# Optimization experiments

Hardware: AMD Instinct MI355X
Metric: run time of the kernel (lower is better)

The kernel has to match this reference:

```python
import jax, jax.numpy as jnp
import numpy as np

B, D, NH, NL, NP, DFF = 2, 256, 8, 4, 4, 1024
HD = D // NH
SHAPES = [(128, 128), (64, 64), (32, 32), (16, 16)]  # (H, W) per level
S = sum(h * w for h, w in SHAPES)  # 21760
EPS = 1e-5


def _layer_norm(x, g, b):
    m = jnp.mean(x, -1, keepdims=True)
    v = jnp.mean(jnp.square(x - m), -1, keepdims=True)
    return (x - m) * jax.lax.rsqrt(v + EPS) * g + b


def _bilinear(v, grid, Hl, Wl):
    # v: [B, Hl*Wl, NH, HD]; grid: [B, S, NH, NP, 2] in [0,1] (x,y)
    # grid_sample semantics, align_corners=False, zero padding
    x = grid[..., 0] * Wl - 0.5
    y = grid[..., 1] * Hl - 0.5
    x0 = jnp.floor(x); y0 = jnp.floor(y)
    dx = x - x0; dy = y - y0
    x0i = x0.astype(jnp.int32); y0i = y0.astype(jnp.int32)

    def corner(xi, yi, w):
        valid = (xi >= 0) & (xi < Wl) & (yi >= 0) & (yi < Hl)
        idx = jnp.clip(yi, 0, Hl - 1) * Wl + jnp.clip(xi, 0, Wl - 1)  # [B,S,NH,NP]
        g_hw = lambda vb, ib: vb[ib]  # [HW,HD],[S,NP] -> [S,NP,HD]
        gat = jax.vmap(jax.vmap(g_hw, in_axes=(1, 1), out_axes=1))(v, idx)  # [B,S,NH,NP,HD]
        return gat * (w * valid.astype(v.dtype))[..., None]

    return (corner(x0i, y0i, (1 - dx) * (1 - dy))
            + corner(x0i + 1, y0i, dx * (1 - dy))
            + corner(x0i, y0i + 1, (1 - dx) * dy)
            + corner(x0i + 1, y0i + 1, dx * dy))


def _ms_deform_attn(query, value_in, ref_pts, shapes,
                    W_off, b_off, W_attn, b_attn, W_val, b_val, W_out, b_out):
    Bq, Sq = query.shape[:2]
    value = (value_in @ W_val + b_val).reshape(Bq, Sq, NH, HD)
    off = (query @ W_off + b_off).reshape(Bq, Sq, NH, NL, NP, 2)
    aw = (query @ W_attn + b_attn).reshape(Bq, Sq, NH, NL * NP)
    aw = jax.nn.softmax(aw, axis=-1).reshape(Bq, Sq, NH, NL, NP)
    # offset normalizer is (W, H) per level
    norm = jnp.array([[w, h] for h, w in shapes], dtype=query.dtype)
    loc = ref_pts[:, :, None, :, None, :] + off / norm[None, None, None, :, None, :]
    out = jnp.zeros((Bq, Sq, NH, HD), query.dtype)
    start = 0
    for l, (Hl, Wl) in enumerate(shapes):
        v_l = value[:, start:start + Hl * Wl]
        sampled = _bilinear(v_l, loc[:, :, :, l], Hl, Wl)  # [B,S,NH,NP,HD]
        out = out + jnp.einsum('bqhp,bqhpd->bqhd', aw[:, :, :, l], sampled)
        start += Hl * Wl
    return out.reshape(Bq, Sq, D) @ W_out + b_out


def setup_inputs() -> dict:
    key = jax.random.key(0)
    ks = jax.random.split(key, 16)
    sc = 0.02
    lsi = np.cumsum([0] + [h * w for h, w in SHAPES[:-1]])
    return dict(
        src=jax.random.normal(ks[0], (B, S, D), jnp.float32),
        pos=jax.random.normal(ks[1], (B, S, D), jnp.float32),
        reference_points=jax.random.uniform(ks[2], (B, S, NL, 2), jnp.float32),
        spatial_shapes=jnp.array(SHAPES, jnp.int32),
        level_start_index=jnp.array(lsi, jnp.int32),
        W_off=sc * jax.random.normal(ks[3], (D, NH * NL * NP * 2), jnp.float32),
        b_off=jnp.zeros((NH * NL * NP * 2,), jnp.float32),
        W_attn=sc * jax.random.normal(ks[4], (D, NH * NL * NP), jnp.float32),
        b_attn=jnp.zeros((NH * NL * NP,), jnp.float32),
        W_val=sc * jax.random.normal(ks[5], (D, D), jnp.float32),
        b_val=jnp.zeros((D,), jnp.float32),
        W_out=sc * jax.random.normal(ks[6], (D, D), jnp.float32),
        b_out=jnp.zeros((D,), jnp.float32),
        g1=jnp.ones((D,), jnp.float32), be1=jnp.zeros((D,), jnp.float32),
        W_ff1=sc * jax.random.normal(ks[7], (D, DFF), jnp.float32),
        b_ff1=jnp.zeros((DFF,), jnp.float32),
        W_ff2=sc * jax.random.normal(ks[8], (DFF, D), jnp.float32),
        b_ff2=jnp.zeros((D,), jnp.float32),
        g2=jnp.ones((D,), jnp.float32), be2=jnp.zeros((D,), jnp.float32),
    )


def reference(src, pos, reference_points, spatial_shapes, level_start_index,
              W_off, b_off, W_attn, b_attn, W_val, b_val, W_out, b_out,
              g1, be1, W_ff1, b_ff1, W_ff2, b_ff2, g2, be2):
    # spatial_shapes is static metadata (defines per-level reshapes)
    shapes = [tuple(int(v) for v in row) for row in np.asarray(spatial_shapes)]
    attn = _ms_deform_attn(src + pos, src, reference_points, shapes,
                           W_off, b_off, W_attn, b_attn, W_val, b_val, W_out, b_out)
    x = _layer_norm(src + attn, g1, be1)
    ffn = jax.nn.relu(x @ W_ff1 + b_ff1) @ W_ff2 + b_ff2
    return _layer_norm(x + ffn, g2, be2)
```

## Files before the change

kernel.cpp:

```cpp
#include <hip/hip_runtime.h>
#include <cstdint>
#include <cstddef>

#define B_   2
#define S_   21760
#define M_   (B_ * S_)
#define D_   256
#define DFF_ 1024
#define EPS_ 1e-5f

typedef __attribute__((ext_vector_type(8))) short short8;
typedef __attribute__((ext_vector_type(4))) float f32x4;
typedef __attribute__((ext_vector_type(2))) float f32x2;

__device__ __forceinline__ ushort f2bf(float f) {
    uint x = __float_as_uint(f);
    return (ushort)((x + 0x7fffu + ((x >> 16) & 1u)) >> 16);
}
__device__ __forceinline__ float bf2f(ushort u) {
    return __uint_as_float(((uint)u) << 16);
}

#define CVT_BLOCKS 10880
__global__ __launch_bounds__(256) void prep_all(
    const float* __restrict__ src, const float* __restrict__ pos,
    ushort* __restrict__ sb, ushort* __restrict__ qb,
    const float* __restrict__ Wval, const float* __restrict__ Woff,
    const float* __restrict__ Wattn, const float* __restrict__ Wout,
    const float* __restrict__ Wff1, const float* __restrict__ Wff2,
    const float* __restrict__ boff, const float* __restrict__ battn,
    ushort* __restrict__ WT, float* __restrict__ bias_oa)
{
    if (blockIdx.x < CVT_BLOCKS) {
        const size_t i = ((size_t)blockIdx.x * 256 + threadIdx.x) * 4;
        const float4 s = *(const float4*)(src + i);
        const float4 p = *(const float4*)(pos + i);
        ushort4 so, qo;
        so.x = f2bf(s.x); so.y = f2bf(s.y); so.z = f2bf(s.z); so.w = f2bf(s.w);
        qo.x = f2bf(s.x + p.x); qo.y = f2bf(s.y + p.y);
        qo.z = f2bf(s.z + p.z); qo.w = f2bf(s.w + p.w);
        *(ushort4*)(sb + i) = so;
        *(ushort4*)(qb + i) = qo;
        return;
    }
    const int i = (blockIdx.x - CVT_BLOCKS) * 256 + threadIdx.x;
    if (i < 65536) {
        const int n = i >> 8, k = i & 255;
        WT[i] = f2bf(Wval[(size_t)k * 256 + n]);
    } else if (i < 163840) {
        const int j = i - 65536;
        const int n = j >> 8, k = j & 255;
        WT[i] = (n < 256) ? f2bf(Woff[(size_t)k * 256 + n])
                          : f2bf(Wattn[(size_t)k * 128 + (n - 256)]);
    } else if (i < 229376) {
        const int j = i - 163840;
        const int n = j >> 8, k = j & 255;
        WT[i] = f2bf(Wout[(size_t)k * 256 + n]);
    } else if (i < 491520) {
        const int j = i - 229376;
        const int n = j >> 8, k = j & 255;
        WT[i] = f2bf(Wff1[(size_t)k * 1024 + n]);
    } else if (i < 753664) {
        const int j = i - 491520;
        const int n = j >> 10, k = j & 1023;
        WT[i] = f2bf(Wff2[(size_t)k * 256 + n]);
    } else if (i < 753664 + 384) {
        const int j = i - 753664;
        bias_oa[j] = (j < 256) ? boff[j] : battn[j - 256];
    }
}

__global__ __launch_bounds__(256) void mgemm(
    const ushort* __restrict__ A, const ushort* __restrict__ WT,
    const float* __restrict__ bias, ushort* __restrict__ C,
    int M, int N, int K, int relu, int mode)
{
    __shared__ __align__(16) ushort Als[128 * 64];
    __shared__ __align__(16) ushort Bls[128 * 64];

    const int nwg = gridDim.x;
    const int bid = blockIdx.x;
    const int q8 = nwg >> 3, r8 = nwg & 7;
    const int xcd = bid & 7, blk = bid >> 3;
    const int wg = (xcd < r8 ? xcd * (q8 + 1) : r8 * (q8 + 1) + (xcd - r8) * q8) + blk;
    const int gx = N >> 7;
    const int n0 = (wg % gx) << 7;
    const int m0 = (wg / gx) << 7;

    const int tid = threadIdx.x;
    const int wv = tid >> 6, ln = tid & 63;
    const int wm = wv >> 1, wn = wv & 1;

    const int srow = ln >> 3;
    const int scol = ((ln & 7) ^ srow) * 8;

    f32x4 acc[4][4];
    const f32x4 zz = {0.f, 0.f, 0.f, 0.f};
    #pragma unroll
    for (int i = 0; i < 4; i++)
        #pragma unroll
        for (int j = 0; j < 4; j++) acc[i][j] = zz;

    const int fr = ln & 15, qq = ln >> 4;

    for (int k0 = 0; k0 < K; k0 += 64) {
        __syncthreads();
        #pragma unroll
        for (int r = 0; r < 4; ++r) {
            const int c = r * 4 + wv;
            const ushort* ga = A + (size_t)(m0 + c * 8 + srow) * K + k0 + scol;
            __builtin_amdgcn_global_load_lds(
                (const __attribute__((address_space(1))) uint*)ga,
                (__attribute__((address_space(3))) uint*)(Als + c * 512), 16, 0, 0);
            const ushort* gb = WT + (size_t)(n0 + c * 8 + srow) * K + k0 + scol;
            __builtin_amdgcn_global_load_lds(
                (const __attribute__((address_space(1))) uint*)gb,
                (__attribute__((address_space(3))) uint*)(Bls + c * 512), 16, 0, 0);
        }
        __syncthreads();

        #pragma unroll
        for (int kk = 0; kk < 2; kk++) {
            short8 af[4], bfr[4];
            #pragma unroll
            for (int i = 0; i < 4; i++) {
                const int row = wm * 64 + i * 16 + fr;
                af[i] = *(const short8*)&Als[row * 64 + (((kk * 4 + qq) ^ (row & 7)) * 8)];
            }
            #pragma unroll
            for (int j = 0; j < 4; j++) {
                const int row = wn * 64 + j * 16 + fr;
                bfr[j] = *(const short8*)&Bls[row * 64 + (((kk * 4 + qq) ^ (row & 7)) * 8)];
            }
            #pragma unroll
            for (int i = 0; i < 4; i++)
                #pragma unroll
                for (int j = 0; j < 4; j++)
                    acc[i][j] = __builtin_amdgcn_mfma_f32_16x16x32_bf16(
                        af[i], bfr[j], acc[i][j], 0, 0, 0);
        }
    }

    uint8_t* C8 = (uint8_t*)C;
    const int rq = (ln >> 4) * 4;
    #pragma unroll
    for (int j = 0; j < 4; j++) {
        const int col = n0 + wn * 64 + j * 16 + fr;
        const float bv = bias[col];
        #pragma unroll
        for (int i = 0; i < 4; i++) {
            #pragma unroll
            for (int r = 0; r < 4; r++) {
                const int row = m0 + wm * 64 + i * 16 + rq + r;
                float v = acc[i][j][r] + bv;
                if (relu) v = fmaxf(v, 0.f);
                if (mode == 0) {
                    C[(size_t)row * N + col] = f2bf(v);
                } else {
                    const int bb = (row >= S_) ? 1 : 0;
                    const int loc = row - bb * S_;
                    const int hh = col >> 5, ch = col & 31;
                    const int pk = __builtin_amdgcn_cvt_pk_fp8_f32(v, v, 0, false);
                    C8[((size_t)(bb * 8 + hh) * S_ + loc) * 32 + ch] = (uint8_t)(pk & 0xff);
                }
            }
        }
    }
}

__global__ __launch_bounds__(256) void ln_row(
    const ushort* __restrict__ a16, const ushort* __restrict__ r16,
    const float* __restrict__ g, const float* __restrict__ be,
    float* __restrict__ o32, ushort* __restrict__ o16)
{
    const int wv = threadIdx.x >> 6, ln = threadIdx.x & 63;
    const int row = blockIdx.x * 4 + wv;
    const int col = ln * 4;
    const size_t base = (size_t)row * 256 + col;

    const ushort4 av = *(const ushort4*)(a16 + base);
    const ushort4 rv = *(const ushort4*)(r16 + base);
    float v0 = bf2f(av.x) + bf2f(rv.x);
    float v1 = bf2f(av.y) + bf2f(rv.y);
    float v2 = bf2f(av.z) + bf2f(rv.z);
    float v3 = bf2f(av.w) + bf2f(rv.w);

    float s = v0 + v1 + v2 + v3;
    float s2 = v0 * v0 + v1 * v1 + v2 * v2 + v3 * v3;
    #pragma unroll
    for (int o = 32; o > 0; o >>= 1) {
        s  += __shfl_down(s, o);
        s2 += __shfl_down(s2, o);
    }
    s = __shfl(s, 0);
    s2 = __shfl(s2, 0);
    const float mean = s * (1.f / 256.f);
    const float var = s2 * (1.f / 256.f) - mean * mean;
    const float rstd = rsqrtf(var + EPS_);

    const float4 gv = *(const float4*)(g + col);
    const float4 bv = *(const float4*)(be + col);
    const float o0 = (v0 - mean) * rstd * gv.x + bv.x;
    const float o1 = (v1 - mean) * rstd * gv.y + bv.y;
    const float o2 = (v2 - mean) * rstd * gv.z + bv.z;
    const float o3 = (v3 - mean) * rstd * gv.w + bv.w;

    if (o32) {
        float4 o; o.x = o0; o.y = o1; o.z = o2; o.w = o3;
        *(float4*)(o32 + base) = o;
    } else {
        ushort4 o; o.x = f2bf(o0); o.y = f2bf(o1); o.z = f2bf(o2); o.w = f2bf(o3);
        *(ushort4*)(o16 + base) = o;
    }
}

__global__ __launch_bounds__(256) void sample8(
    const uint8_t* __restrict__ value, const ushort* __restrict__ offaw,
    const float* __restrict__ refp, ushort* __restrict__ samp)
{
    const int bid = blockIdx.x;
    const int wg = (bid & 7) * 680 + (bid >> 3);
    const int bh = wg / 340;
    const int qc = wg - bh * 340;
    const int b = bh >> 3, h = bh & 7;

    const int tid = threadIdx.x;
    const int g = tid >> 2, cg = tid & 3;
    const int q = b * S_ + qc * 64 + g;
    const int half = cg >> 1;
    const int gbase = (tid & 63) & ~3;

    const int Wl = 128 >> cg;
    const float fW = (float)Wl;
    const int st = (cg == 0) ? 0 : (cg == 1) ? 16384 : (cg == 2) ? 20480 : 21504;

    const ushort* awq = offaw + (size_t)q * 384 + 256 + h * 16 + cg * 4;
    const uint2 lg = *(const uint2*)awq;
    const float l0 = bf2f((ushort)(lg.x & 0xffff)), l1 = bf2f((ushort)(lg.x >> 16));
    const float l2 = bf2f((ushort)(lg.y & 0xffff)), l3 = bf2f((ushort)(lg.y >> 16));
    float mx = fmaxf(fmaxf(l0, l1), fmaxf(l2, l3));
    mx = fmaxf(mx, __shfl_xor(mx, 1));
    mx = fmaxf(mx, __shfl_xor(mx, 2));
    const float e0 = __expf(l0 - mx), e1 = __expf(l1 - mx);
    const float e2 = __expf(l2 - mx), e3 = __expf(l3 - mx);
    float sm = e0 + e1 + e2 + e3;
    sm += __shfl_xor(sm, 1);
    sm += __shfl_xor(sm, 2);
    const float inv = 1.f / sm;
    const float aj[4] = {e0 * inv, e1 * inv, e2 * inv, e3 * inv};

    const ushort* ofq = offaw + (size_t)q * 384 + h * 32 + cg * 8;
    const uint4 of = *(const uint4*)ofq;
    const uint ou[4] = {of.x, of.y, of.z, of.w};
    const float rx = refp[(size_t)q * 8 + cg * 2];
    const float ry = refp[(size_t)q * 8 + cg * 2 + 1];

    int  rxo[8];
    uint wpk[8];
    #pragma unroll
    for (int j = 0; j < 4; j++) {
        const float ox = bf2f((ushort)(ou[j] & 0xffff));
        const float oy = bf2f((ushort)(ou[j] >> 16));
        const float x = fmaf(rx, fW, ox) - 0.5f;
        const float y = fmaf(ry, fW, oy) - 0.5f;
        const float fx0 = floorf(x), fy0 = floorf(y);
        const float dx = x - fx0, dy = y - fy0;
        const int x0 = (int)fx0, y0 = (int)fy0;

        const int bx = min(max(x0, 0), Wl - 2);
        const float mwx0 = ((x0 >= 0) & (x0 < Wl)) ? (1.f - dx) : 0.f;
        const float mwx1 = ((x0 + 1 >= 0) & (x0 + 1 < Wl)) ? dx : 0.f;
        const int xc0 = min(max(x0, 0), Wl - 1);
        const int xc1 = min(max(x0 + 1, 0), Wl - 1);
        const float wAx = (xc0 == bx ? mwx0 : 0.f) + (xc1 == bx ? mwx1 : 0.f);
        const float wBx = (xc0 == bx + 1 ? mwx0 : 0.f) + (xc1 == bx + 1 ? mwx1 : 0.f);

        const int yc0 = min(max(y0, 0), Wl - 1);
        const int yc1 = min(max(y0 + 1, 0), Wl - 1);
        const float mwy0 = ((y0 >= 0) & (y0 < Wl)) ? (1.f - dy) : 0.f;
        const float mwy1 = ((y0 + 1 >= 0) & (y0 + 1 < Wl)) ? dy : 0.f;

        const float a = aj[j];
        rxo[2 * j]     = (st + yc0 * Wl + bx) * 32;
        rxo[2 * j + 1] = (st + yc1 * Wl + bx) * 32;
        wpk[2 * j]     = (uint)f2bf(a * wAx * mwy0) | ((uint)f2bf(a * wBx * mwy0) << 16);
        wpk[2 * j + 1] = (uint)f2bf(a * wAx * mwy1) | ((uint)f2bf(a * wBx * mwy1) << 16);
    }

    const uint8_t* vb = value + (size_t)(b * 8 + h) * S_ * 32 + cg * 16;
    f32x2 acc[8];
    #pragma unroll
    for (int k = 0; k < 8; k++) acc[k] = (f32x2){0.f, 0.f};

    #pragma unroll
    for (int ol = 0; ol < 4; ol++) {
        const int srcl = gbase + ol;
        #pragma unroll
        for (int r = 0; r < 8; r++) {
            const int  rix = __shfl(rxo[r], srcl, 64);
            const uint wp  = (uint)__shfl((int)wpk[r], srcl, 64);
            const float wv = bf2f((ushort)(half ? (wp >> 16) : (wp & 0xffffu)));
            const uint4 u = *(const uint4*)(vb + rix);
            const f32x2 w2 = {wv, wv};
            acc[0] += w2 * __builtin_amdgcn_cvt_pk_f32_fp8((int)u.x, false);
            acc[1] += w2 * __builtin_amdgcn_cvt_pk_f32_fp8((int)u.x, true);
            acc[2] += w2 * __builtin_amdgcn_cvt_pk_f32_fp8((int)u.y, false);
            acc[3] += w2 * __builtin_amdgcn_cvt_pk_f32_fp8((int)u.y, true);
            acc[4] += w2 * __builtin_amdgcn_cvt_pk_f32_fp8((int)u.z, false);
            acc[5] += w2 * __builtin_amdgcn_cvt_pk_f32_fp8((int)u.z, true);
            acc[6] += w2 * __builtin_amdgcn_cvt_pk_f32_fp8((int)u.w, false);
            acc[7] += w2 * __builtin_amdgcn_cvt_pk_f32_fp8((int)u.w, true);
        }
    }

    #pragma unroll
    for (int k = 0; k < 8; k++) {
        acc[k].x += __shfl_xor(acc[k].x, 2);
        acc[k].y += __shfl_xor(acc[k].y, 2);
    }

    f32x2 r0, r1, r2, r3;
    if (half == 0) { r0 = acc[0]; r1 = acc[1]; r2 = acc[2]; r3 = acc[3]; }
    else           { r0 = acc[4]; r1 = acc[5]; r2 = acc[6]; r3 = acc[7]; }

    const int ch_start = (cg & 1) * 16 + half * 8;
    uint4 o;
    o.x = (uint)f2bf(r0.x) | ((uint)f2bf(r0.y) << 16);
    o.y = (uint)f2bf(r1.x) | ((uint)f2bf(r1.y) << 16);
    o.z = (uint)f2bf(r2.x) | ((uint)f2bf(r2.y) << 16);
    o.w = (uint)f2bf(r3.x) | ((uint)f2bf(r3.y) << 16);
    *(uint4*)(samp + (size_t)q * 256 + h * 32 + ch_start) = o;
}

extern "C" void kernel_launch(void* const* d_in, const int* in_sizes, int n_in,
                              void* d_out, int out_size, void* d_ws, size_t ws_size,
                              hipStream_t stream)
{
    const float* src    = (const float*)d_in[0];
    const float* pos    = (const float*)d_in[1];
    const float* refp   = (const float*)d_in[2];
    const float* W_off  = (const float*)d_in[5];
    const float* b_off  = (const float*)d_in[6];
    const float* W_attn = (const float*)d_in[7];
    const float* b_attn = (const float*)d_in[8];
    const float* W_val  = (const float*)d_in[9];
    const float* b_val  = (const float*)d_in[10];
    const float* W_out  = (const float*)d_in[11];
    const float* b_out  = (const float*)d_in[12];
    const float* g1     = (const float*)d_in[13];
    const float* be1    = (const float*)d_in[14];
    const float* W_ff1  = (const float*)d_in[15];
    const float* b_ff1  = (const float*)d_in[16];
    const float* W_ff2  = (const float*)d_in[17];
    const float* b_ff2  = (const float*)d_in[18];
    const float* g2     = (const float*)d_in[19];
    const float* be2    = (const float*)d_in[20];
    float* out = (float*)d_out;

    const size_t szMDh = (size_t)M_ * 256 * 2;
    const size_t szOAh = (size_t)M_ * 384 * 2;

    char* ws = (char*)d_ws;
    ushort* WT      = (ushort*)ws;
    ushort* WT_val  = WT;
    ushort* WT_oa   = WT + 65536;
    ushort* WT_out  = WT + 163840;
    ushort* WT_ff1  = WT + 229376;
    ushort* WT_ff2  = WT + 491520;
    float*  bias_oa = (float*)(ws + 1507328);

    const size_t o_src  = 2097152;
    const size_t o_q    = o_src + szMDh;
    const size_t o_val  = o_q   + szMDh;
    const size_t o_oa   = o_val + szMDh;
    const size_t o_x    = o_oa  + szOAh;
    const size_t o_ffn  = o_x   + szMDh;

    ushort* src_bf  = (ushort*)(ws + o_src);
    ushort* q_bf    = (ushort*)(ws + o_q);
    ushort* val_f8  = (ushort*)(ws + o_val);
    ushort* offaw   = (ushort*)(ws + o_oa);
    ushort* x_bf    = (ushort*)(ws + o_x);
    ushort* ffn_bf  = (ushort*)(ws + o_ffn);
    ushort* samp_bf = q_bf;
    ushort* attn_bf = val_f8;
    ushort* hbuf    = src_bf;

    prep_all<<<CVT_BLOCKS + 2947, 256, 0, stream>>>(
        src, pos, src_bf, q_bf,
        W_val, W_off, W_attn, W_out, W_ff1, W_ff2, b_off, b_attn, WT, bias_oa);
    mgemm<<<2 * (M_ / 128), 256, 0, stream>>>(src_bf, WT_val, b_val, val_f8, M_, 256, 256, 0, 2);
    mgemm<<<3 * (M_ / 128), 256, 0, stream>>>(q_bf, WT_oa, bias_oa, offaw, M_, 384, 256, 0, 0);
    sample8<<<16 * 340, 256, 0, stream>>>((const uint8_t*)val_f8, offaw, refp, samp_bf);
    mgemm<<<2 * (M_ / 128), 256, 0, stream>>>(samp_bf, WT_out, b_out, attn_bf, M_, 256, 256, 0, 0);
    ln_row<<<M_ / 4, 256, 0, stream>>>(attn_bf, src_bf, g1, be1, nullptr, x_bf);
    mgemm<<<8 * (M_ / 128), 256, 0, stream>>>(x_bf, WT_ff1, b_ff1, hbuf, M_, DFF_, 256, 1, 0);
    mgemm<<<2 * (M_ / 128), 256, 0, stream>>>(hbuf, WT_ff2, b_ff2, ffn_bf, M_, 256, DFF_, 0, 0);
    ln_row<<<M_ / 4, 256, 0, stream>>>(ffn_bf, x_bf, g2, be2, out, nullptr);
}
```

Baseline: 249.6 us.

## Run output projection and FFN2 GEMMs in FP8 with swizzled layouts

Adds an FP8 MFMA GEMM kernel (16x16x32 fp8) with XOR-swizzled K layout to avoid LDS bank conflicts. The sampler now writes FP8 outputs, the FFN1 GEMM writes its ReLU activations as swizzled FP8, and the W_out and W_ff2 weights are pre-converted to swizzled FP8. This halves activation traffic and doubles MFMA throughput for the out-projection and FFN2 GEMMs, at the cost of reduced numerical precision.

```diff
diff --git a/kernel.cpp b/kernel.cpp
--- a/kernel.cpp
+++ b/kernel.cpp
@@ -19,6 +19,12 @@
 }
 __device__ __forceinline__ float bf2f(ushort u) {
     return __uint_as_float(((uint)u) << 16);
+}
+__device__ __forceinline__ uint8_t f2f8(float v) {
+    return (uint8_t)(__builtin_amdgcn_cvt_pk_fp8_f32(v, v, 0, false) & 0xff);
+}
+__device__ __forceinline__ int kswz(int c, int row) {
+    return (c & ~63) | ((((c >> 4) & 3) ^ (row & 3)) << 4) | (c & 15);
 }
 
 #define CVT_BLOCKS 10880
@@ -29,7 +35,8 @@
     const float* __restrict__ Wattn, const float* __restrict__ Wout,
     const float* __restrict__ Wff1, const float* __restrict__ Wff2,
     const float* __restrict__ boff, const float* __restrict__ battn,
-    ushort* __restrict__ WT, float* __restrict__ bias_oa)
+    ushort* __restrict__ WT, uint8_t* __restrict__ WT8,
+    float* __restrict__ bias_oa)
 {
     if (blockIdx.x < CVT_BLOCKS) {
         const size_t i = ((size_t)blockIdx.x * 256 + threadIdx.x) * 4;
@@ -52,18 +59,18 @@
         const int n = j >> 8, k = j & 255;
         WT[i] = (n < 256) ? f2bf(Woff[(size_t)k * 256 + n])
                           : f2bf(Wattn[(size_t)k * 128 + (n - 256)]);
-    } else if (i < 229376) {
+    } else if (i < 425984) {
         const int j = i - 163840;
         const int n = j >> 8, k = j & 255;
-        WT[i] = f2bf(Wout[(size_t)k * 256 + n]);
+        WT[i] = f2bf(Wff1[(size_t)k * 1024 + n]);
     } else if (i < 491520) {
-        const int j = i - 229376;
+        const int j = i - 425984;
         const int n = j >> 8, k = j & 255;
-        WT[i] = f2bf(Wff1[(size_t)k * 1024 + n]);
+        WT8[(size_t)n * 256 + kswz(k, n)] = f2f8(Wout[(size_t)k * 256 + n]);
     } else if (i < 753664) {
         const int j = i - 491520;
         const int n = j >> 10, k = j & 1023;
-        WT[i] = f2bf(Wff2[(size_t)k * 256 + n]);
+        WT8[65536 + (size_t)n * 1024 + kswz(k, n)] = f2f8(Wff2[(size_t)k * 256 + n]);
     } else if (i < 753664 + 384) {
         const int j = i - 753664;
         bias_oa[j] = (j < 256) ? boff[j] : battn[j - 256];
@@ -156,13 +163,100 @@
                 if (relu) v = fmaxf(v, 0.f);
                 if (mode == 0) {
                     C[(size_t)row * N + col] = f2bf(v);
-                } else {
+                } else if (mode == 2) {
                     const int bb = (row >= S_) ? 1 : 0;
                     const int loc = row - bb * S_;
                     const int hh = col >> 5, ch = col & 31;
-                    const int pk = __builtin_amdgcn_cvt_pk_fp8_f32(v, v, 0, false);
-                    C8[((size_t)(bb * 8 + hh) * S_ + loc) * 32 + ch] = (uint8_t)(pk & 0xff);
+                    C8[((size_t)(bb * 8 + hh) * S_ + loc) * 32 + ch] = f2f8(v);
+                } else {
+                    C8[(size_t)row * N + kswz(col, row)] = f2f8(v);
                 }
+            }
+        }
+    }
+}
+
+__global__ __launch_bounds__(256) void mgemm8(
+    const uint8_t* __restrict__ A, const uint8_t* __restrict__ W8,
+    const float* __restrict__ bias, ushort* __restrict__ C,
+    int M, int N, int K)
+{
+    __shared__ __align__(16) uint8_t Als[128 * 64];
+    __shared__ __align__(16) uint8_t Bls[128 * 64];
+
+    const int nwg = gridDim.x;
+    const int bid = blockIdx.x;
+    const int q8 = nwg >> 3, r8 = nwg & 7;
+    const int xcd = bid & 7, blk = bid >> 3;
+    const int wg = (xcd < r8 ? xcd * (q8 + 1) : r8 * (q8 + 1) + (xcd - r8) * q8) + blk;
+    const int gx = N >> 7;
+    const int n0 = (wg % gx) << 7;
+    const int m0 = (wg / gx) << 7;
+
+    const int tid = threadIdx.x;
+    const int wv = tid >> 6, ln = tid & 63;
+    const int wm = wv >> 1, wn = wv & 1;
+    const int fr = ln & 15, qq = ln >> 4;
+
+    f32x4 acc[4][4];
+    const f32x4 zz = {0.f, 0.f, 0.f, 0.f};
+    #pragma unroll
+    for (int i = 0; i < 4; i++)
+        #pragma unroll
+        for (int j = 0; j < 4; j++) acc[i][j] = zz;
+
+    for (int k0 = 0; k0 < K; k0 += 64) {
+        __syncthreads();
+        #pragma unroll
+        for (int r = 0; r < 2; ++r) {
+            const int row = r * 64 + (tid >> 2);
+            const int sl = (tid & 3) * 16;
+            const uint8_t* ga = A + (size_t)(m0 + row) * K + k0 + sl;
+            __builtin_amdgcn_global_load_lds(
+                (const __attribute__((address_space(1))) uint*)ga,
+                (__attribute__((address_space(3))) uint*)(Als + row * 64 + sl), 16, 0, 0);
+            const uint8_t* gb = W8 + (size_t)(n0 + row) * K + k0 + sl;
+            __builtin_amdgcn_global_load_lds(
+                (const __attribute__((address_space(1))) uint*)gb,
+                (__attribute__((address_space(3))) uint*)(Bls + row * 64 + sl), 16, 0, 0);
+        }
+        __syncthreads();
+
+        #pragma unroll
+        for (int kk = 0; kk < 2; kk++) {
+            long af[4], bfr[4];
+            #pragma unroll
+            for (int i = 0; i < 4; i++) {
+                const int row = wm * 64 + i * 16 + fr;
+                af[i] = *(const long*)&Als[row * 64 +
+                        ((((kk * 2 + (qq >> 1)) ^ (row & 3)) << 4) | ((qq & 1) * 8))];
+            }
+            #pragma unroll
+            for (int j = 0; j < 4; j++) {
+                const int row = wn * 64 + j * 16 + fr;
+                bfr[j] = *(const long*)&Bls[row * 64 +
+                        ((((kk * 2 + (qq >> 1)) ^ (row & 3)) << 4) | ((qq & 1) * 8))];
+            }
+            #pragma unroll
+            for (int i = 0; i < 4; i++)
+                #pragma unroll
+                for (int j = 0; j < 4; j++)
+                    acc[i][j] = __builtin_amdgcn_mfma_f32_16x16x32_fp8_fp8(
+                        af[i], bfr[j], acc[i][j], 0, 0, 0);
+        }
+    }
+
+    const int rq = (ln >> 4) * 4;
+    #pragma unroll
+    for (int j = 0; j < 4; j++) {
+        const int col = n0 + wn * 64 + j * 16 + fr;
+        const float bv = bias[col];
+        #pragma unroll
+        for (int i = 0; i < 4; i++) {
+            #pragma unroll
+            for (int r = 0; r < 4; r++) {
+                const int row = m0 + wm * 64 + i * 16 + rq + r;
+                C[(size_t)row * N + col] = f2bf(acc[i][j][r] + bv);
             }
         }
     }
@@ -216,7 +310,7 @@
 
 __global__ __launch_bounds__(256) void sample8(
     const uint8_t* __restrict__ value, const ushort* __restrict__ offaw,
-    const float* __restrict__ refp, ushort* __restrict__ samp)
+    const float* __restrict__ refp, uint8_t* __restrict__ samp8)
 {
     const int bid = blockIdx.x;
     const int wg = (bid & 7) * 680 + (bid >> 3);
@@ -323,13 +417,15 @@
     if (half == 0) { r0 = acc[0]; r1 = acc[1]; r2 = acc[2]; r3 = acc[3]; }
     else           { r0 = acc[4]; r1 = acc[5]; r2 = acc[6]; r3 = acc[7]; }
 
-    const int ch_start = (cg & 1) * 16 + half * 8;
-    uint4 o;
-    o.x = (uint)f2bf(r0.x) | ((uint)f2bf(r0.y) << 16);
-    o.y = (uint)f2bf(r1.x) | ((uint)f2bf(r1.y) << 16);
-    o.z = (uint)f2bf(r2.x) | ((uint)f2bf(r2.y) << 16);
-    o.w = (uint)f2bf(r3.x) | ((uint)f2bf(r3.y) << 16);
-    *(uint4*)(samp + (size_t)q * 256 + h * 32 + ch_start) = o;
+    const uint p0 = (uint)__builtin_amdgcn_cvt_pk_fp8_f32(r0.x, r0.y, 0, false);
+    const uint p1 = (uint)__builtin_amdgcn_cvt_pk_fp8_f32(r1.x, r1.y, 0, false);
+    const uint p2 = (uint)__builtin_amdgcn_cvt_pk_fp8_f32(r2.x, r2.y, 0, false);
+    const uint p3 = (uint)__builtin_amdgcn_cvt_pk_fp8_f32(r3.x, r3.y, 0, false);
+    uint2 o8;
+    o8.x = (p0 & 0xffffu) | (p1 << 16);
+    o8.y = (p2 & 0xffffu) | (p3 << 16);
+    const int c = h * 32 + (cg & 1) * 16 + half * 8;
+    *(uint2*)(samp8 + (size_t)q * 256 + kswz(c, q)) = o8;
 }
 
 extern "C" void kernel_launch(void* const* d_in, const int* in_sizes, int n_in,
@@ -361,13 +457,14 @@
     const size_t szOAh = (size_t)M_ * 384 * 2;
 
     char* ws = (char*)d_ws;
-    ushort* WT      = (ushort*)ws;
-    ushort* WT_val  = WT;
-    ushort* WT_oa   = WT + 65536;
-    ushort* WT_out  = WT + 163840;
-    ushort* WT_ff1  = WT + 229376;
-    ushort* WT_ff2  = WT + 491520;
-    float*  bias_oa = (float*)(ws + 1507328);
+    ushort*  WT      = (ushort*)ws;
+    ushort*  WT_val  = WT;
+    ushort*  WT_oa   = WT + 65536;
+    ushort*  WT_ff1  = WT + 163840;
+    uint8_t* WT8     = (uint8_t*)(ws + 851968);
+    uint8_t* WT8_out = WT8;
+    uint8_t* WT8_ff2 = WT8 + 65536;
+    float*   bias_oa = (float*)(ws + 1507328);
 
     const size_t o_src  = 2097152;
     const size_t o_q    = o_src + szMDh;
@@ -376,25 +473,26 @@
     const size_t o_x    = o_oa  + szOAh;
     const size_t o_ffn  = o_x   + szMDh;
 
-    ushort* src_bf  = (ushort*)(ws + o_src);
-    ushort* q_bf    = (ushort*)(ws + o_q);
-    ushort* val_f8  = (ushort*)(ws + o_val);
-    ushort* offaw   = (ushort*)(ws + o_oa);
-    ushort* x_bf    = (ushort*)(ws + o_x);
-    ushort* ffn_bf  = (ushort*)(ws + o_ffn);
-    ushort* samp_bf = q_bf;
-    ushort* attn_bf = val_f8;
-    ushort* hbuf    = src_bf;
+    ushort*  src_bf = (ushort*)(ws + o_src);
+    ushort*  q_bf   = (ushort*)(ws + o_q);
+    ushort*  val_f8 = (ushort*)(ws + o_val);
+    ushort*  offaw  = (ushort*)(ws + o_oa);
+    ushort*  x_bf   = (ushort*)(ws + o_x);
+    ushort*  ffn_bf = (ushort*)(ws + o_ffn);
+    uint8_t* samp8  = (uint8_t*)q_bf;
+    ushort*  attn_bf = val_f8;
+    uint8_t* h8     = (uint8_t*)src_bf;
 
     prep_all<<<CVT_BLOCKS + 2947, 256, 0, stream>>>(
         src, pos, src_bf, q_bf,
-        W_val, W_off, W_attn, W_out, W_ff1, W_ff2, b_off, b_attn, WT, bias_oa);
+        W_val, W_off, W_attn, W_out, W_ff1, W_ff2, b_off, b_attn,
+        WT, WT8, bias_oa);
     mgemm<<<2 * (M_ / 128), 256, 0, stream>>>(src_bf, WT_val, b_val, val_f8, M_, 256, 256, 0, 2);
     mgemm<<<3 * (M_ / 128), 256, 0, stream>>>(q_bf, WT_oa, bias_oa, offaw, M_, 384, 256, 0, 0);
-    sample8<<<16 * 340, 256, 0, stream>>>((const uint8_t*)val_f8, offaw, refp, samp_bf);
-    mgemm<<<2 * (M_ / 128), 256, 0, stream>>>(samp_bf, WT_out, b_out, attn_bf, M_, 256, 256, 0, 0);
+    sample8<<<16 * 340, 256, 0, stream>>>((const uint8_t*)val_f8, offaw, refp, samp8);
+    mgemm8<<<2 * (M_ / 128), 256, 0, stream>>>(samp8, WT8_out, b_out, attn_bf, M_, 256, 256);
     ln_row<<<M_ / 4, 256, 0, stream>>>(attn_bf, src_bf, g1, be1, nullptr, x_bf);
-    mgemm<<<8 * (M_ / 128), 256, 0, stream>>>(x_bf, WT_ff1, b_ff1, hbuf, M_, DFF_, 256, 1, 0);
-    mgemm<<<2 * (M_ / 128), 256, 0, stream>>>(hbuf, WT_ff2, b_ff2, ffn_bf, M_, 256, DFF_, 0, 0);
+    mgemm<<<8 * (M_ / 128), 256, 0, stream>>>(x_bf, WT_ff1, b_ff1, (ushort*)h8, M_, DFF_, 256, 1, 3);
+    mgemm8<<<2 * (M_ / 128), 256, 0, stream>>>(h8, WT8_ff2, b_ff2, ffn_bf, M_, 256, DFF_);
     ln_row<<<M_ / 4, 256, 0, stream>>>(ffn_bf, x_bf, g2, be2, out, nullptr);
 }
```

New measurement: 268.1 us. 7.4% more time.
